# Kernel optimization log

Measured on AMD Instinct MI355X. Metric: run time of the kernel, lower is better.

## Reference

```python
import jax, jax.numpy as jnp
import numpy as np

N = 100000          # num_nodes
E = 1_600_000       # num_edges
F = 16              # node_features
HID = 32            # DCRNN hidden size (hardcoded in DCRNNModel)
OUT = 12            # output_len
K = 2               # diffusion steps (intended DCRNN; see notes)
CIN = F + HID       # DConv input channels: concat([X, H])


def setup_inputs() -> dict:
    key = jax.random.key(0)
    ks = jax.random.split(key, 12)
    x = jax.random.normal(ks[0], (N, F), dtype=jnp.float32)
    edge_index = jax.random.randint(ks[1], (2, E), 0, N, dtype=jnp.int32)
    edge_weight = jax.random.uniform(ks[2], (E,), jnp.float32, minval=0.05, maxval=1.0)
    sc = 0.1
    W_z = jax.random.normal(ks[3], (2, K, CIN, HID), jnp.float32) * sc
    b_z = jax.random.normal(ks[4], (HID,), jnp.float32) * sc
    W_r = jax.random.normal(ks[5], (2, K, CIN, HID), jnp.float32) * sc
    b_r = jax.random.normal(ks[6], (HID,), jnp.float32) * sc
    W_h = jax.random.normal(ks[7], (2, K, CIN, HID), jnp.float32) * sc
    b_h = jax.random.normal(ks[8], (HID,), jnp.float32) * sc
    lin_W = jax.random.normal(ks[9], (HID, OUT), jnp.float32) * sc
    lin_b = jax.random.normal(ks[10], (OUT,), jnp.float32) * sc
    return {"x": x, "edge_index": edge_index, "edge_weight": edge_weight,
            "W_z": W_z, "b_z": b_z, "W_r": W_r, "b_r": b_r,
            "W_h": W_h, "b_h": b_h, "lin_W": lin_W, "lin_b": lin_b}


def reference(x, edge_index, edge_weight, W_z, b_z, W_r, b_r, W_h, b_h, lin_W, lin_b):
    src, dst = edge_index[0], edge_index[1]
    # weighted out/in degrees (as in to_dense_adj row/col sums)
    deg_out = jax.ops.segment_sum(edge_weight, src, num_segments=N)
    deg_in = jax.ops.segment_sum(edge_weight, dst, num_segments=N)
    inv_out_e = (1.0 / deg_out)[src][:, None]  # [E,1] per-edge 1/deg_out(src)
    inv_in_e = (1.0 / deg_in)[dst][:, None]    # [E,1] per-edge 1/deg_in(dst)

    def dconv(Xc, W, b):
        # K=0 term (both diffusion directions share Tx_0 = X)
        H = Xc @ W[0, 0] + Xc @ W[1, 0]
        # forward diffusion: out[dst] += (1/deg_out[src]) * Xc[src]
        T_o = jax.ops.segment_sum(inv_out_e * Xc[src], dst, num_segments=N)
        # reverse diffusion: out[src] += (1/deg_in[dst]) * Xc[dst]
        T_i = jax.ops.segment_sum(inv_in_e * Xc[dst], src, num_segments=N)
        return H + T_o @ W[0, 1] + T_i @ W[1, 1] + b

    H0 = jnp.zeros((N, HID), dtype=x.dtype)
    XH = jnp.concatenate([x, H0], axis=1)           # [N, F+HID]
    Z = jax.nn.sigmoid(dconv(XH, W_z, b_z))         # update gate
    R = jax.nn.sigmoid(dconv(XH, W_r, b_r))         # reset gate
    XHr = jnp.concatenate([x, H0 * R], axis=1)
    H_tilde = jnp.tanh(dconv(XHr, W_h, b_h))
    H = Z * H0 + (1.0 - Z) * H_tilde                # [N, HID]
    return jax.nn.relu(H) @ lin_W + lin_b           # [N, OUT]
```

## Files before the change

### kernel.cpp

```cpp
#include <hip/hip_runtime.h>
#include <math.h>

#define N_NODES 100000
#define N_EDGES 1600000
#define NF 16
#define HID 32
#define OUTD 12
#define CIN3 48

#define NB   1024
#define RNG  98
#define PBLK 256
#define PT   1024
#define CHUNK ((N_EDGES + PBLK - 1) / PBLK)

typedef unsigned int uint;


__global__ __launch_bounds__(PT)
void p1_count(const int* __restrict__ ei, uint* __restrict__ cntD, uint* __restrict__ cntS) {
    __shared__ uint cD[NB], cS[NB];
    int t = threadIdx.x, blk = blockIdx.x;
    for (int i = t; i < NB; i += PT) { cD[i] = 0; cS[i] = 0; }
    __syncthreads();
    int lo = blk * CHUNK, hi = min(lo + CHUNK, N_EDGES);
    for (int e = lo + t; e < hi; e += PT) {
        uint s = (uint)ei[e];
        uint d = (uint)ei[N_EDGES + e];
        atomicAdd(&cS[s / RNG], 1u);
        atomicAdd(&cD[d / RNG], 1u);
    }
    __syncthreads();
    for (int i = t; i < NB; i += PT) {
        cntD[i * PBLK + blk] = cD[i];
        cntS[i * PBLK + blk] = cS[i];
    }
}

__global__ __launch_bounds__(256)
void p2a_rowsum(const uint* __restrict__ cntD, const uint* __restrict__ cntS,
                uint* __restrict__ totD, uint* __restrict__ totS) {
    __shared__ uint red[256];
    int t = threadIdx.x;
    bool isS = blockIdx.x >= NB;
    int b = isS ? (blockIdx.x - NB) : blockIdx.x;
    const uint* cnt = isS ? cntS : cntD;
    red[t] = cnt[b * PBLK + t];
    __syncthreads();
    for (int s = 128; s > 0; s >>= 1) { if (t < s) red[t] += red[t + s]; __syncthreads(); }
    if (t == 0) (isS ? totS : totD)[b] = red[0];
}

__global__ __launch_bounds__(256)
void p2b_scan(const uint* __restrict__ totD, const uint* __restrict__ totS,
              uint* __restrict__ baseD, uint* __restrict__ baseS) {
    __shared__ uint part[256];
    int t = threadIdx.x;
    for (int dir = 0; dir < 2; ++dir) {
        const uint* tot = dir ? totS : totD;
        uint* base = dir ? baseS : baseD;
        uint v[4]; uint s = 0;
#pragma unroll
        for (int k = 0; k < 4; ++k) { v[k] = tot[t * 4 + k]; s += v[k]; }
        part[t] = s;
        __syncthreads();
        if (t == 0) {
            uint a = 0;
            for (int k = 0; k < 256; ++k) { uint x = part[k]; part[k] = a; a += x; }
            base[NB] = a;
        }
        __syncthreads();
        uint a = part[t];
#pragma unroll
        for (int k = 0; k < 4; ++k) { base[t * 4 + k] = a; a += v[k]; }
        __syncthreads();
    }
}

__global__ __launch_bounds__(256)
void p2c_rowscan(const uint* __restrict__ cntD, const uint* __restrict__ cntS,
                 const uint* __restrict__ baseD, const uint* __restrict__ baseS,
                 uint* __restrict__ offD, uint* __restrict__ offS) {
    __shared__ uint row[PBLK];
    int t = threadIdx.x;
    bool isS = blockIdx.x >= NB;
    int b = isS ? (blockIdx.x - NB) : blockIdx.x;
    const uint* cnt = isS ? cntS : cntD;
    const uint* base = isS ? baseS : baseD;
    uint* off = isS ? offS : offD;
    row[t] = cnt[b * PBLK + t];
    __syncthreads();
    if (t == 0) {
        uint a = base[b];
        for (int k = 0; k < PBLK; ++k) { uint v = row[k]; row[k] = a; a += v; }
    }
    __syncthreads();
    off[b * PBLK + t] = row[t];
}

__global__ __launch_bounds__(PT)
void p3_scatter(const int* __restrict__ ei, const float* __restrict__ ew,
                const uint* __restrict__ cntD, const uint* __restrict__ cntS,
                const uint* __restrict__ offD, const uint* __restrict__ offS,
                uint* __restrict__ recXD, uint* __restrict__ recWD,
                uint* __restrict__ recXS, uint* __restrict__ recWS) {
    __shared__ uint sorted[CHUNK];
    __shared__ uint sbuf[NB];
    __shared__ uint cstart[NB];
    __shared__ uint scur[NB];
    int t = threadIdx.x, blk = blockIdx.x;
    int lo = blk * CHUNK, hi = min(lo + CHUNK, N_EDGES);
    int n = hi - lo;

    for (int dir = 0; dir < 2; ++dir) {
        const uint* cnt = dir ? cntS : cntD;
        const uint* off = dir ? offS : offD;
        uint* recX      = dir ? recXS : recXD;
        uint* recW      = dir ? recWS : recWD;
        const int* own  = dir ? ei : (ei + N_EDGES);
        uint v = cnt[t * PBLK + blk];
        sbuf[t] = v;
        __syncthreads();
        for (int d = 1; d < NB; d <<= 1) {
            uint a = (t >= d) ? sbuf[t - d] : 0u;
            __syncthreads();
            sbuf[t] += a;
            __syncthreads();
        }
        cstart[t] = sbuf[t] - v;
        scur[t]   = sbuf[t] - v;
        __syncthreads();
        sbuf[t] = off[t * PBLK + blk];
        for (int i = t; i < n; i += PT) {
            uint b = (uint)own[lo + i] / RNG;
            uint p = atomicAdd(&scur[b], 1u);
            sorted[p] = (b << 13) | (uint)i;
        }
        __syncthreads();
        for (int i = t; i < n; i += PT) {
            uint v2 = sorted[i];
            uint b = v2 >> 13;
            int e = lo + (int)(v2 & 8191u);
            uint s  = (uint)ei[e];
            uint d2 = (uint)ei[N_EDGES + e];
            uint wfix = (uint)(ew[e] * 16777216.0f + 0.5f);
            uint ownode = dir ? s : d2;
            uint other  = dir ? d2 : s;
            uint lcl  = ownode - b * RNG;
            uint gpos = sbuf[b] + (i - cstart[b]);
            recX[gpos] = other | (lcl << 20);
            recW[gpos] = (lcl << 25) | wfix;
        }
        __syncthreads();
    }
}

__global__ __launch_bounds__(256)
void kdeg(const uint* __restrict__ recWD, const uint* __restrict__ recWS,
          const uint* __restrict__ baseD, const uint* __restrict__ baseS,
          float* __restrict__ inv_in, float* __restrict__ inv_out) {
    __shared__ uint dacc[RNG];
    int t = threadIdx.x;
    bool isS = blockIdx.x >= NB;
    int b = isS ? (blockIdx.x - NB) : blockIdx.x;
    const uint* rec = isS ? recWS : recWD;
    const uint* base = isS ? baseS : baseD;
    float* inv = isS ? inv_out : inv_in;
    for (int i = t; i < RNG; i += 256) dacc[i] = 0u;
    __syncthreads();
    uint lo = base[b], hi = base[b + 1];
    for (uint e = lo + t; e < hi; e += 256) {
        uint r = rec[e];
        atomicAdd(&dacc[r >> 25], r & 0x1FFFFFFu);
    }
    __syncthreads();
    int n0 = b * RNG;
    for (int i = t; i < RNG; i += 256) {
        int n = n0 + i;
        if (n < N_NODES) inv[n] = 16777216.0f / (float)dacc[i];
    }
}

__global__ __launch_bounds__(256)
void p4_fixed(const uint* __restrict__ recXD, const uint* __restrict__ recXS,
              const uint* __restrict__ baseD, const uint* __restrict__ baseS,
              const float* __restrict__ x,
              const float* __restrict__ inv_out, const float* __restrict__ inv_in,
              float* __restrict__ To, float* __restrict__ Ti) {
    __shared__ uint dacc[RNG * NF];
    int t = threadIdx.x;
    bool isS = blockIdx.x >= NB;
    int b = isS ? (blockIdx.x - NB) : blockIdx.x;
    const uint* rec = isS ? recXS : recXD;
    const uint* base = isS ? baseS : baseD;
    const float* inv = isS ? inv_in : inv_out;
    float* out = isS ? Ti : To;
    for (int i = t; i < RNG * NF; i += 256) dacc[i] = 0u;
    __syncthreads();
    uint lo = base[b], hi = base[b + 1];
    int f = t & 15, g = t >> 4;
    uint e = lo + g;
    for (; e + 112 < hi; e += 128) {
        uint r[8];
#pragma unroll
        for (int k = 0; k < 8; ++k) r[k] = rec[e + 16 * k];
        float v[8];
#pragma unroll
        for (int k = 0; k < 8; ++k) {
            uint o = r[k] & 0xFFFFFu;
            v[k] = x[(size_t)o * NF + f] * inv[o];
        }
#pragma unroll
        for (int k = 0; k < 8; ++k)
            atomicAdd(&dacc[(r[k] >> 20) * NF + f],
                      (uint)__float2int_rn(v[k] * 1048576.0f));
    }
    for (; e < hi; e += 16) {
        uint r = rec[e];
        uint o = r & 0xFFFFFu;
        float v = x[(size_t)o * NF + f] * inv[o];
        atomicAdd(&dacc[(r >> 20) * NF + f], (uint)__float2int_rn(v * 1048576.0f));
    }
    __syncthreads();
    size_t o0 = (size_t)b * RNG * NF;
    int lim = N_NODES * NF - (int)o0;
    for (int i = t; i < RNG * NF; i += 256)
        if (i < lim) out[o0 + i] = (float)(int)dacc[i] * (1.0f / 1048576.0f);
}

__global__ void wprep_kernel(const float* __restrict__ Wz, const float* __restrict__ Wh,
                             float* __restrict__ WzT, float* __restrict__ WhT) {
    int t = blockIdx.x * blockDim.x + threadIdx.x;
    if (t >= 2 * CIN3 * HID) return;
    const float* W = (t < CIN3 * HID) ? Wz : Wh;
    float* WT      = (t < CIN3 * HID) ? WzT : WhT;
    int i = (t < CIN3 * HID) ? t : (t - CIN3 * HID);
    int c = i / HID;
    int h = i - c * HID;
    float v;
    if (c < 16)      v = W[(0 * 48 + c) * 32 + h] + W[(2 * 48 + c) * 32 + h];
    else if (c < 32) v = W[(1 * 48 + (c - 16)) * 32 + h];
    else             v = W[(3 * 48 + (c - 32)) * 32 + h];
    WT[h * CIN3 + c] = v;
}

__global__ __launch_bounds__(256)
void node_kernel(const float* __restrict__ x, const float* __restrict__ To,
                 const float* __restrict__ Ti,
                 const float* __restrict__ WzT, const float* __restrict__ WhT,
                 const float* __restrict__ bz, const float* __restrict__ bh,
                 const float* __restrict__ linW, const float* __restrict__ linb,
                 float* __restrict__ out) {
    __shared__ __align__(16) float sWz[HID * CIN3];
    __shared__ __align__(16) float sWh[HID * CIN3];
    __shared__ __align__(16) float sBz[HID], sBh[HID];
    __shared__ __align__(16) float sLW[HID * OUTD];
    __shared__ __align__(16) float sLb[OUTD];

    for (int i = threadIdx.x; i < HID * CIN3; i += 256) { sWz[i] = WzT[i]; sWh[i] = WhT[i]; }
    if (threadIdx.x < HID) { sBz[threadIdx.x] = bz[threadIdx.x]; sBh[threadIdx.x] = bh[threadIdx.x]; }
    for (int i = threadIdx.x; i < HID * OUTD; i += 256) sLW[i] = linW[i];
    if (threadIdx.x < OUTD) sLb[threadIdx.x] = linb[threadIdx.x];
    __syncthreads();

    int n = blockIdx.x * 256 + threadIdx.x;
    if (n >= N_NODES) return;

    float feat[CIN3];
#pragma unroll
    for (int q = 0; q < 4; ++q) {
        float4 v = ((const float4*)(x + (size_t)n * NF))[q];
        feat[q*4+0]=v.x; feat[q*4+1]=v.y; feat[q*4+2]=v.z; feat[q*4+3]=v.w;
    }
#pragma unroll
    for (int q = 0; q < 4; ++q) {
        float4 v = ((const float4*)(To + (size_t)n * NF))[q];
        feat[16+q*4+0]=v.x; feat[16+q*4+1]=v.y; feat[16+q*4+2]=v.z; feat[16+q*4+3]=v.w;
    }
#pragma unroll
    for (int q = 0; q < 4; ++q) {
        float4 v = ((const float4*)(Ti + (size_t)n * NF))[q];
        feat[32+q*4+0]=v.x; feat[32+q*4+1]=v.y; feat[32+q*4+2]=v.z; feat[32+q*4+3]=v.w;
    }

    float o[OUTD];
#pragma unroll
    for (int j = 0; j < OUTD; ++j) o[j] = sLb[j];

#pragma unroll 2
    for (int h = 0; h < HID; ++h) {
        float az = sBz[h];
        float ah = sBh[h];
        const float4* wz4 = (const float4*)(sWz + h * CIN3);
        const float4* wh4 = (const float4*)(sWh + h * CIN3);
#pragma unroll
        for (int q = 0; q < CIN3 / 4; ++q) {
            float4 wz = wz4[q];
            float4 wh = wh4[q];
            float f0 = feat[q*4+0], f1 = feat[q*4+1], f2 = feat[q*4+2], f3 = feat[q*4+3];
            az += f0*wz.x + f1*wz.y + f2*wz.z + f3*wz.w;
            ah += f0*wh.x + f1*wh.y + f2*wh.z + f3*wh.w;
        }
        float z  = 1.0f / (1.0f + expf(-az));
        float ht = tanhf(ah);
        float r  = fmaxf((1.0f - z) * ht, 0.0f);
#pragma unroll
        for (int j = 0; j < OUTD; ++j) o[j] += r * sLW[h * OUTD + j];
    }

    float4* op = (float4*)(out + (size_t)n * OUTD);
    op[0] = make_float4(o[0], o[1], o[2],  o[3]);
    op[1] = make_float4(o[4], o[5], o[6],  o[7]);
    op[2] = make_float4(o[8], o[9], o[10], o[11]);
}

__global__ void zero_kernel(float* __restrict__ p, int n) {
    int i = blockIdx.x * blockDim.x + threadIdx.x;
    int stride = gridDim.x * blockDim.x;
    for (; i < n; i += stride) p[i] = 0.0f;
}
__global__ void degree_compact(const int* __restrict__ ei, const float* __restrict__ ew,
                               float* __restrict__ deg_out, float* __restrict__ deg_in) {
    int e = blockIdx.x * blockDim.x + threadIdx.x;
    if (e >= N_EDGES) return;
    atomicAdd(&deg_out[ei[e]], ew[e]);
    atomicAdd(&deg_in[ei[N_EDGES + e]], ew[e]);
}
__global__ void rcp_compact(float* __restrict__ a, float* __restrict__ b) {
    int n = blockIdx.x * blockDim.x + threadIdx.x;
    if (n >= N_NODES) return;
    a[n] = 1.0f / a[n]; b[n] = 1.0f / b[n];
}
__global__ __launch_bounds__(256)
void scatter_kernel(const int* __restrict__ ei, const float* __restrict__ x,
                    const float* __restrict__ inv_out, const float* __restrict__ inv_in,
                    float* __restrict__ To, float* __restrict__ Ti) {
    int t = blockIdx.x * blockDim.x + threadIdx.x;
    if (t >= N_EDGES * NF) return;
    int e = t >> 4, f = t & 15;
    int src = ei[e], dst = ei[N_EDGES + e];
    atomicAdd(&To[dst * NF + f], x[src * NF + f] * inv_out[src]);
    atomicAdd(&Ti[src * NF + f], x[dst * NF + f] * inv_in[dst]);
}

extern "C" void kernel_launch(void* const* d_in, const int* in_sizes, int n_in,
                              void* d_out, int out_size, void* d_ws, size_t ws_size,
                              hipStream_t stream) {
    const float* x    = (const float*)d_in[0];
    const int*   ei   = (const int*)  d_in[1];
    const float* ew   = (const float*)d_in[2];
    const float* Wz   = (const float*)d_in[3];
    const float* bz   = (const float*)d_in[4];
    const float* Wh   = (const float*)d_in[7];
    const float* bh   = (const float*)d_in[8];
    const float* linW = (const float*)d_in[9];
    const float* linb = (const float*)d_in[10];

    float* ws = (float*)d_ws;

    size_t off = 0;
    uint* recXD = (uint*)(ws + off);  off += (size_t)N_EDGES;
    uint* recWD = (uint*)(ws + off);  off += (size_t)N_EDGES;
    uint* recXS = (uint*)(ws + off);  off += (size_t)N_EDGES;
    uint* recWS = (uint*)(ws + off);  off += (size_t)N_EDGES;
    uint* cntD  = (uint*)(ws + off);  off += (size_t)NB * PBLK;
    uint* cntS  = (uint*)(ws + off);  off += (size_t)NB * PBLK;
    uint* offD  = (uint*)(ws + off);  off += (size_t)NB * PBLK;
    uint* offS  = (uint*)(ws + off);  off += (size_t)NB * PBLK;
    uint* totD  = (uint*)(ws + off);  off += NB;
    uint* totS  = (uint*)(ws + off);  off += NB;
    uint* baseD = (uint*)(ws + off);  off += NB + 1;
    uint* baseS = (uint*)(ws + off);  off += NB + 1;
    float* inv_out = ws + off;        off += N_NODES;
    float* inv_in  = ws + off;        off += N_NODES;
    float* To   = ws + off;           off += (size_t)NF * N_NODES;
    float* Ti   = ws + off;           off += (size_t)NF * N_NODES;
    float* WzT  = ws + off;           off += CIN3 * HID;
    float* WhT  = ws + off;           off += CIN3 * HID;
    size_t need = off * sizeof(float);

    if (ws_size >= need) {
        p1_count    <<<PBLK,  PT,  0, stream>>>(ei, cntD, cntS);
        p2a_rowsum  <<<2*NB,  256, 0, stream>>>(cntD, cntS, totD, totS);
        p2b_scan    <<<1,     256, 0, stream>>>(totD, totS, baseD, baseS);
        p2c_rowscan <<<2*NB,  256, 0, stream>>>(cntD, cntS, baseD, baseS, offD, offS);
        p3_scatter  <<<PBLK,  PT,  0, stream>>>(ei, ew, cntD, cntS, offD, offS,
                                                recXD, recWD, recXS, recWS);
        kdeg        <<<2*NB,  256, 0, stream>>>(recWD, recWS, baseD, baseS, inv_in, inv_out);
        wprep_kernel<<<12,    256, 0, stream>>>(Wz, Wh, WzT, WhT);
        p4_fixed    <<<2*NB,  256, 0, stream>>>(recXD, recXS, baseD, baseS, x,
                                                inv_out, inv_in, To, Ti);
        node_kernel <<<(N_NODES + 255) / 256, 256, 0, stream>>>(x, To, Ti, WzT, WhT, bz, bh,
                                                                linW, linb, (float*)d_out);
    } else {
        float* fTo  = ws;
        float* fTi  = ws + 16 * N_NODES;
        float* fIo  = ws + 32 * N_NODES;
        float* fIi  = ws + 33 * N_NODES;
        float* fWzT = ws + 34 * N_NODES;
        float* fWhT = fWzT + CIN3 * HID;
        zero_kernel<<<2048, 256, 0, stream>>>(fTo, 34 * N_NODES);
        degree_compact<<<(N_EDGES + 255) / 256, 256, 0, stream>>>(ei, ew, fIo, fIi);
        rcp_compact<<<(N_NODES + 255) / 256, 256, 0, stream>>>(fIo, fIi);
        scatter_kernel<<<(N_EDGES * NF + 255) / 256, 256, 0, stream>>>(ei, x, fIo, fIi, fTo, fTi);
        wprep_kernel<<<12, 256, 0, stream>>>(Wz, Wh, fWzT, fWhT);
        node_kernel<<<(N_NODES + 255) / 256, 256, 0, stream>>>(x, fTo, fTi, fWzT, fWhT, bz, bh,
                                                               linW, linb, (float*)d_out);
    }
}
```

Baseline: 162.3 us.

## Prescale node features into bf16 tables and fold weight prep into node kernel

Result: faster. 156.4 us (-3.6%).

```diff
diff --git a/kernel.cpp b/kernel.cpp
--- a/kernel.cpp
+++ b/kernel.cpp
@@ -15,6 +15,7 @@
 #define CHUNK ((N_EDGES + PBLK - 1) / PBLK)
 
 typedef unsigned int uint;
+typedef unsigned short ushort;
 
 
 __global__ __launch_bounds__(PT)
@@ -156,36 +157,52 @@
 }
 
 __global__ __launch_bounds__(256)
-void kdeg(const uint* __restrict__ recWD, const uint* __restrict__ recWS,
-          const uint* __restrict__ baseD, const uint* __restrict__ baseS,
-          float* __restrict__ inv_in, float* __restrict__ inv_out) {
-    __shared__ uint dacc[RNG];
-    int t = threadIdx.x;
-    bool isS = blockIdx.x >= NB;
-    int b = isS ? (blockIdx.x - NB) : blockIdx.x;
-    const uint* rec = isS ? recWS : recWD;
-    const uint* base = isS ? baseS : baseD;
-    float* inv = isS ? inv_out : inv_in;
-    for (int i = t; i < RNG; i += 256) dacc[i] = 0u;
-    __syncthreads();
-    uint lo = base[b], hi = base[b + 1];
+void kdeg2(const uint* __restrict__ recWD, const uint* __restrict__ recWS,
+           const uint* __restrict__ baseD, const uint* __restrict__ baseS,
+           const float* __restrict__ x,
+           ushort* __restrict__ xs, ushort* __restrict__ xd) {
+    __shared__ uint daccI[RNG], daccO[RNG];
+    __shared__ float invI[RNG], invO[RNG];
+    int t = threadIdx.x, b = blockIdx.x;
+    for (int i = t; i < RNG; i += 256) { daccI[i] = 0u; daccO[i] = 0u; }
+    __syncthreads();
+    uint lo = baseD[b], hi = baseD[b + 1];
     for (uint e = lo + t; e < hi; e += 256) {
-        uint r = rec[e];
-        atomicAdd(&dacc[r >> 25], r & 0x1FFFFFFu);
-    }
-    __syncthreads();
-    int n0 = b * RNG;
+        uint r = recWD[e];
+        atomicAdd(&daccI[r >> 25], r & 0x1FFFFFFu);
+    }
+    lo = baseS[b]; hi = baseS[b + 1];
+    for (uint e = lo + t; e < hi; e += 256) {
+        uint r = recWS[e];
+        atomicAdd(&daccO[r >> 25], r & 0x1FFFFFFu);
+    }
+    __syncthreads();
     for (int i = t; i < RNG; i += 256) {
-        int n = n0 + i;
-        if (n < N_NODES) inv[n] = 16777216.0f / (float)dacc[i];
+        invI[i] = 16777216.0f / (float)daccI[i];
+        invO[i] = 16777216.0f / (float)daccO[i];
+    }
+    __syncthreads();
+    int base = b * RNG * NF;
+    int lim = N_NODES * NF - base;
+    for (int i = t; i < RNG * NF; i += 256) {
+        if (i < lim) {
+            int nl = i >> 4;
+            float v = x[base + i];
+            float a = v * invO[nl];
+            float c = v * invI[nl];
+            uint u;
+            u = __float_as_uint(a); u += 0x7FFFu + ((u >> 16) & 1u);
+            xs[base + i] = (ushort)(u >> 16);
+            u = __float_as_uint(c); u += 0x7FFFu + ((u >> 16) & 1u);
+            xd[base + i] = (ushort)(u >> 16);
+        }
     }
 }
 
 __global__ __launch_bounds__(256)
 void p4_fixed(const uint* __restrict__ recXD, const uint* __restrict__ recXS,
               const uint* __restrict__ baseD, const uint* __restrict__ baseS,
-              const float* __restrict__ x,
-              const float* __restrict__ inv_out, const float* __restrict__ inv_in,
+              const ushort* __restrict__ xs, const ushort* __restrict__ xd,
               float* __restrict__ To, float* __restrict__ Ti) {
     __shared__ uint dacc[RNG * NF];
     int t = threadIdx.x;
@@ -193,7 +210,7 @@
     int b = isS ? (blockIdx.x - NB) : blockIdx.x;
     const uint* rec = isS ? recXS : recXD;
     const uint* base = isS ? baseS : baseD;
-    const float* inv = isS ? inv_in : inv_out;
+    const ushort* src = isS ? xd : xs;
     float* out = isS ? Ti : To;
     for (int i = t; i < RNG * NF; i += 256) dacc[i] = 0u;
     __syncthreads();
@@ -208,7 +225,7 @@
 #pragma unroll
         for (int k = 0; k < 8; ++k) {
             uint o = r[k] & 0xFFFFFu;
-            v[k] = x[(size_t)o * NF + f] * inv[o];
+            v[k] = __uint_as_float((uint)src[(size_t)o * NF + f] << 16);
         }
 #pragma unroll
         for (int k = 0; k < 8; ++k)
@@ -218,7 +235,7 @@
     for (; e < hi; e += 16) {
         uint r = rec[e];
         uint o = r & 0xFFFFFu;
-        float v = x[(size_t)o * NF + f] * inv[o];
+        float v = __uint_as_float((uint)src[(size_t)o * NF + f] << 16);
         atomicAdd(&dacc[(r >> 20) * NF + f], (uint)__float2int_rn(v * 1048576.0f));
     }
     __syncthreads();
@@ -228,26 +245,10 @@
         if (i < lim) out[o0 + i] = (float)(int)dacc[i] * (1.0f / 1048576.0f);
 }
 
-__global__ void wprep_kernel(const float* __restrict__ Wz, const float* __restrict__ Wh,
-                             float* __restrict__ WzT, float* __restrict__ WhT) {
-    int t = blockIdx.x * blockDim.x + threadIdx.x;
-    if (t >= 2 * CIN3 * HID) return;
-    const float* W = (t < CIN3 * HID) ? Wz : Wh;
-    float* WT      = (t < CIN3 * HID) ? WzT : WhT;
-    int i = (t < CIN3 * HID) ? t : (t - CIN3 * HID);
-    int c = i / HID;
-    int h = i - c * HID;
-    float v;
-    if (c < 16)      v = W[(0 * 48 + c) * 32 + h] + W[(2 * 48 + c) * 32 + h];
-    else if (c < 32) v = W[(1 * 48 + (c - 16)) * 32 + h];
-    else             v = W[(3 * 48 + (c - 32)) * 32 + h];
-    WT[h * CIN3 + c] = v;
-}
-
 __global__ __launch_bounds__(256)
 void node_kernel(const float* __restrict__ x, const float* __restrict__ To,
                  const float* __restrict__ Ti,
-                 const float* __restrict__ WzT, const float* __restrict__ WhT,
+                 const float* __restrict__ Wz, const float* __restrict__ Wh,
                  const float* __restrict__ bz, const float* __restrict__ bh,
                  const float* __restrict__ linW, const float* __restrict__ linb,
                  float* __restrict__ out) {
@@ -257,7 +258,21 @@
     __shared__ __align__(16) float sLW[HID * OUTD];
     __shared__ __align__(16) float sLb[OUTD];
 
-    for (int i = threadIdx.x; i < HID * CIN3; i += 256) { sWz[i] = WzT[i]; sWh[i] = WhT[i]; }
+    for (int i = threadIdx.x; i < HID * CIN3; i += 256) {
+        int h = i / CIN3, c = i - h * CIN3;
+        float vz, vh;
+        if (c < 16) {
+            vz = Wz[(0 * 48 + c) * 32 + h] + Wz[(2 * 48 + c) * 32 + h];
+            vh = Wh[(0 * 48 + c) * 32 + h] + Wh[(2 * 48 + c) * 32 + h];
+        } else if (c < 32) {
+            vz = Wz[(1 * 48 + (c - 16)) * 32 + h];
+            vh = Wh[(1 * 48 + (c - 16)) * 32 + h];
+        } else {
+            vz = Wz[(3 * 48 + (c - 32)) * 32 + h];
+            vh = Wh[(3 * 48 + (c - 32)) * 32 + h];
+        }
+        sWz[i] = vz; sWh[i] = vh;
+    }
     if (threadIdx.x < HID) { sBz[threadIdx.x] = bz[threadIdx.x]; sBh[threadIdx.x] = bh[threadIdx.x]; }
     for (int i = threadIdx.x; i < HID * OUTD; i += 256) sLW[i] = linW[i];
     if (threadIdx.x < OUTD) sLb[threadIdx.x] = linb[threadIdx.x];
@@ -371,12 +386,10 @@
     uint* totS  = (uint*)(ws + off);  off += NB;
     uint* baseD = (uint*)(ws + off);  off += NB + 1;
     uint* baseS = (uint*)(ws + off);  off += NB + 1;
-    float* inv_out = ws + off;        off += N_NODES;
-    float* inv_in  = ws + off;        off += N_NODES;
+    ushort* xs  = (ushort*)(ws + off); off += (size_t)N_NODES * NF / 2;
+    ushort* xd  = (ushort*)(ws + off); off += (size_t)N_NODES * NF / 2;
     float* To   = ws + off;           off += (size_t)NF * N_NODES;
     float* Ti   = ws + off;           off += (size_t)NF * N_NODES;
-    float* WzT  = ws + off;           off += CIN3 * HID;
-    float* WhT  = ws + off;           off += CIN3 * HID;
     size_t need = off * sizeof(float);
 
     if (ws_size >= need) {
@@ -386,25 +399,20 @@
         p2c_rowscan <<<2*NB,  256, 0, stream>>>(cntD, cntS, baseD, baseS, offD, offS);
         p3_scatter  <<<PBLK,  PT,  0, stream>>>(ei, ew, cntD, cntS, offD, offS,
                                                 recXD, recWD, recXS, recWS);
-        kdeg        <<<2*NB,  256, 0, stream>>>(recWD, recWS, baseD, baseS, inv_in, inv_out);
-        wprep_kernel<<<12,    256, 0, stream>>>(Wz, Wh, WzT, WhT);
-        p4_fixed    <<<2*NB,  256, 0, stream>>>(recXD, recXS, baseD, baseS, x,
-                                                inv_out, inv_in, To, Ti);
-        node_kernel <<<(N_NODES + 255) / 256, 256, 0, stream>>>(x, To, Ti, WzT, WhT, bz, bh,
+        kdeg2       <<<NB,    256, 0, stream>>>(recWD, recWS, baseD, baseS, x, xs, xd);
+        p4_fixed    <<<2*NB,  256, 0, stream>>>(recXD, recXS, baseD, baseS, xs, xd, To, Ti);
+        node_kernel <<<(N_NODES + 255) / 256, 256, 0, stream>>>(x, To, Ti, Wz, Wh, bz, bh,
                                                                 linW, linb, (float*)d_out);
     } else {
         float* fTo  = ws;
         float* fTi  = ws + 16 * N_NODES;
         float* fIo  = ws + 32 * N_NODES;
         float* fIi  = ws + 33 * N_NODES;
-        float* fWzT = ws + 34 * N_NODES;
-        float* fWhT = fWzT + CIN3 * HID;
         zero_kernel<<<2048, 256, 0, stream>>>(fTo, 34 * N_NODES);
         degree_compact<<<(N_EDGES + 255) / 256, 256, 0, stream>>>(ei, ew, fIo, fIi);
         rcp_compact<<<(N_NODES + 255) / 256, 256, 0, stream>>>(fIo, fIi);
         scatter_kernel<<<(N_EDGES * NF + 255) / 256, 256, 0, stream>>>(ei, x, fIo, fIi, fTo, fTi);
-        wprep_kernel<<<12, 256, 0, stream>>>(Wz, Wh, fWzT, fWhT);
-        node_kernel<<<(N_NODES + 255) / 256, 256, 0, stream>>>(x, fTo, fTi, fWzT, fWhT, bz, bh,
+        node_kernel<<<(N_NODES + 255) / 256, 256, 0, stream>>>(x, fTo, fTi, Wz, Wh, bz, bh,
                                                                linW, linb, (float*)d_out);
     }
 }
```
